# Optimization experiments

Hardware: AMD Instinct MI355X
Metric: run time of the kernel (lower is better)

The kernel has to match this reference:

```python
import jax, jax.numpy as jnp
import numpy as np

VOCAB_BLOCK = 2048
TEMP = 1.0
EPS_LO = 0.2
EPS_HI = 0.3


def setup_inputs() -> dict:
    key = jax.random.key(0)
    k = jax.random.split(key, 6)
    B, S, D, V = 4, 1024, 2048, 32768
    hidden_states = jax.random.normal(k[0], (B, S, D), dtype=jnp.float32)
    # 0.02 init scale keeps logits O(1) so exp/logsumexp stay well-conditioned
    lm_head_kernel = jax.random.normal(k[1], (D, V), dtype=jnp.float32) * 0.02
    input_ids = jax.random.randint(k[2], (B, S), 0, V, dtype=jnp.int32)
    labels = jax.random.randint(k[3], (B, S), 0, 2, dtype=jnp.int32)
    advantages = jax.random.normal(k[4], (B,), dtype=jnp.float32)
    old_per_token_logps = jax.random.normal(k[5], (B, S - 1), dtype=jnp.float32) * 0.1
    return {
        "hidden_states": hidden_states,
        "lm_head_kernel": lm_head_kernel,
        "input_ids": input_ids,
        "labels": labels,
        "advantages": advantages,
        "old_per_token_logps": old_per_token_logps,
    }


def _fused_logps(h, kernel):
    """Streaming logsumexp over vocab blocks; never materializes [B,T,V]."""
    B, T, D = h.shape
    V = kernel.shape[1]
    nb = V // VOCAB_BLOCK
    Wb = kernel.reshape(D, nb, VOCAB_BLOCK).transpose(1, 0, 2)  # [nb, D, bs]

    def step(carry, wb):
        m, s = carry
        lg = jnp.einsum("btd,dv->btv", h, wb) / TEMP  # [B,T,bs]
        bm = lg.max(axis=-1)
        nm = jnp.maximum(m, bm)
        s = s * jnp.exp(m - nm) + jnp.exp(lg - nm[..., None]).sum(axis=-1)
        return (nm, s), None

    init = (jnp.full((B, T), -jnp.inf, dtype=h.dtype), jnp.zeros((B, T), dtype=h.dtype))
    (m, s), _ = jax.lax.scan(step, init, Wb)
    return m + jnp.log(s)  # logsumexp over full vocab, [B,T]


def reference(hidden_states, lm_head_kernel, input_ids, labels, advantages, old_per_token_logps):
    h = hidden_states[:, :-1, :]            # [B,T,D], T = S-1
    chosen = input_ids[:, 1:]               # [B,T]
    mask = labels[:, 1:].astype(jnp.float32)

    # chosen-token logit: gather kernel columns, no full logits tensor
    w_sel = lm_head_kernel.T[chosen]        # [B,T,D]
    chosen_logit = jnp.einsum("btd,btd->bt", h, w_sel) / TEMP

    lse = _fused_logps(h, lm_head_kernel)
    per_token_logps = chosen_logit - lse    # [B,T]

    ratio = jnp.exp(per_token_logps - old_per_token_logps)
    adv = advantages[:, None]
    loss1 = ratio * adv
    loss2 = jnp.clip(ratio, 1.0 - EPS_LO, 1.0 + EPS_HI) * adv
    per_token_loss = -jnp.minimum(loss1, loss2)

    total_valid = mask.sum()
    loss = (per_token_loss * mask).sum() / total_valid
    return loss, jax.lax.stop_gradient(per_token_logps)
```

## Files before the change

### kernel.cpp

```cpp
#include <hip/hip_runtime.h>
#include <hip/hip_bf16.h>

typedef unsigned short u16;
typedef unsigned char u8;
typedef unsigned long long u64;
typedef __attribute__((ext_vector_type(4))) int i32x4;
typedef __attribute__((ext_vector_type(8))) int i32x8;
typedef __attribute__((ext_vector_type(4))) float f32x4;

#define NROWS 4092
#define NROWS_PAD 4096
#define DDIM 2048
#define VDIM 32768
#define NCHUNK 512
#define SC8 0x7F7F7F7F
#define BUFB 65536u

__device__ __forceinline__ u8 f2fp8(float f) {
  union { float f; unsigned u; } v; v.f = f;
  unsigned s = (v.u >> 24) & 0x80u;
  unsigned a = v.u & 0x7FFFFFFFu;
  if (a >= 0x43E80000u) return (u8)(s | 0x7E);
  int e = (int)(a >> 23) - 127;
  unsigned m = a & 0x7FFFFFu;
  if (e < -6) {
    unsigned full = m | 0x800000u;
    int sh = 20 + (-6 - e);
    if (sh > 31) return (u8)s;
    unsigned q = full >> sh;
    unsigned rem = full & ((1u << sh) - 1u), half = 1u << (sh - 1);
    q += (rem > half || (rem == half && (q & 1u)));
    return (u8)(s | q);
  }
  unsigned q = m >> 20, rem = m & 0xFFFFFu;
  q += (rem > 0x80000u || (rem == 0x80000u && (q & 1u)));
  unsigned bits = (((unsigned)(e + 7)) << 3) + q;
  if (bits >= 0x7Fu) bits = 0x7Eu;
  return (u8)(s | bits);
}

__device__ __forceinline__ void gload16(const void* g, void* l) {
  using gp_t = const __attribute__((address_space(1))) unsigned*;
  using lp_t = __attribute__((address_space(3))) unsigned*;
  __builtin_amdgcn_global_load_lds((gp_t)g, (lp_t)(unsigned)(unsigned long long)l,
                                   16, 0, 0);
}

#define BAR() __builtin_amdgcn_s_barrier()
#define SB()  __builtin_amdgcn_sched_barrier(0)
#define SHUF(a, b) __builtin_shufflevector(a, b, 0, 1, 2, 3, 4, 5, 6, 7)

__global__ void init_k(const int* __restrict__ ids, int* __restrict__ chosen,
                       float* __restrict__ chlog, float* __restrict__ accum) {
  int i = blockIdx.x * 256 + threadIdx.x;
  if (i < NROWS_PAD) {
    int v = -1;
    if (i < NROWS) { int b = i / 1023, t = i % 1023; v = ids[b * 1024 + t + 1]; }
    chosen[i] = v;
    chlog[i] = 0.f;
  }
  if (i < 2) accum[i] = 0.f;
}

__global__ void bucket_k(const int* __restrict__ chosen,
                         int* __restrict__ boff, int* __restrict__ bent) {
  __shared__ int cnt[512];
  __shared__ int base[512];
  int tid = threadIdx.x;
  cnt[tid] = 0;
  __syncthreads();
  int loc[8], tile[8];
#pragma unroll
  for (int j = 0; j < 8; ++j) {
    int r = tid + (j << 9);
    int c = chosen[r];
    int ti = (c < 0) ? 512 : (c >> 6);
    tile[j] = ti;
    loc[j] = (ti < 512) ? atomicAdd(&cnt[ti], 1) : 0;
  }
  __syncthreads();
  if (tid == 0) {
    int s = 0;
    for (int i = 0; i < 512; ++i) { base[i] = s; s += cnt[i]; }
  }
  __syncthreads();
  boff[tid] = base[tid];
  if (tid == 511) boff[512] = base[511] + cnt[511];
#pragma unroll
  for (int j = 0; j < 8; ++j) {
    int r = tid + (j << 9);
    if (tile[j] < 512) bent[base[tile[j]] + loc[j]] = (r << 6) | (chosen[r] & 63);
  }
}

__global__ void conv_h(const float* __restrict__ hs, u8* __restrict__ h8) {
  int idx = blockIdx.x * 256 + threadIdx.x;
  int row = idx >> 8;
  int c8 = (idx & 255) << 3;
  u64 o = 0;
  if (row < NROWS) {
    int b = row / 1023, t = row % 1023;
    const float* p = hs + (size_t)((b << 10) + t) * DDIM + c8;
    float4 x = *(const float4*)p, y = *(const float4*)(p + 4);
    o = (u64)f2fp8(x.x * 16.f)        | ((u64)f2fp8(x.y * 16.f) << 8) |
        ((u64)f2fp8(x.z * 16.f) << 16) | ((u64)f2fp8(x.w * 16.f) << 24) |
        ((u64)f2fp8(y.x * 16.f) << 32) | ((u64)f2fp8(y.y * 16.f) << 40) |
        ((u64)f2fp8(y.z * 16.f) << 48) | ((u64)f2fp8(y.w * 16.f) << 56);
  }
  *(u64*)(h8 + (size_t)row * DDIM + c8) = o;
}

__global__ void transpose_w(const float* __restrict__ W, u8* __restrict__ WT8,
                            const float* __restrict__ hs,
                            const int* __restrict__ boff,
                            const int* __restrict__ bent,
                            float* __restrict__ chlog) {
  __shared__ __align__(16) float t32[64][68];
  __shared__ __align__(16) u8 t8[64][68];
  int v0 = blockIdx.x << 6, d0 = blockIdx.y << 6;
  int tid = threadIdx.x;
  int vi = (tid & 15) << 2, dl = tid >> 4;
#pragma unroll
  for (int i = 0; i < 4; ++i) {
    int d = dl + (i << 4);
    float4 w = *(const float4*)(W + (size_t)(d0 + d) * VDIM + v0 + vi);
    *(float4*)&t32[d][vi] = w;
    unsigned p = (unsigned)f2fp8(w.x * 64.f) |
                 ((unsigned)f2fp8(w.y * 64.f) << 8) |
                 ((unsigned)f2fp8(w.z * 64.f) << 16) |
                 ((unsigned)f2fp8(w.w * 64.f) << 24);
    *(unsigned*)&t8[d][vi] = p;
  }
  __syncthreads();
  int m0 = boff[blockIdx.x], m1 = boff[blockIdx.x + 1];
  int lane = tid & 63, wv = tid >> 6;
  for (int m = m0 + wv; m < m1; m += 4) {
    int e = bent[m];
    int r = e >> 6, cv = e & 63;
    int b = r / 1023, tt = r % 1023;
    float s = hs[(size_t)((b << 10) + tt) * DDIM + d0 + lane] * t32[lane][cv];
#pragma unroll
    for (int o = 1; o < 64; o <<= 1) s += __shfl_xor(s, o, 64);
    if (lane == 0) atomicAdd(chlog + r, s);
  }
  int vr = tid >> 2, dc = (tid & 3) << 4;
  union { u8 b[16]; ulonglong2 q; } u;
#pragma unroll
  for (int k = 0; k < 16; ++k) u.b[k] = t8[dc + k][vr];
  *(ulonglong2*)(WT8 + (size_t)(v0 + vr) * DDIM + d0 + dc) = u.q;
}

__global__ __launch_bounds__(512, 2) void gemm_lse(
    const u8* __restrict__ A, const u8* __restrict__ Bt,
    float2* __restrict__ partials) {
  extern __shared__ u16 smem[];
  char* lds = (char*)smem;

  const int tid = threadIdx.x;
  const int l = tid & 63;
  const int wid = tid >> 6;
  const int wm = wid >> 2, wn = wid & 3;
  const int ln = l & 15;
  const int g4 = l >> 4;
  const int xr = ln & 7;

  int bid = blockIdx.x;
  int id = ((bid & 7) << 8) | (bid >> 3);
  int bm = id & 15;
  int bn = id >> 4;
  const int m0 = bm << 8, n0 = bn << 8;

  const u8* Ab = A + (size_t)m0 * DDIM;
  const u8* Bb = Bt + (size_t)n0 * DDIM;

  const unsigned aA0 = (unsigned)((wm << 14) + (ln << 7)) + (((0 | g4) ^ xr) << 4);
  const unsigned aA1 = (unsigned)((wm << 14) + (ln << 7)) + (((4 | g4) ^ xr) << 4);
  const unsigned aB0 = 32768u + (unsigned)((wn << 13) + (ln << 7)) + (((0 | g4) ^ xr) << 4);
  const unsigned aB1 = 32768u + (unsigned)((wn << 13) + (ln << 7)) + (((4 | g4) ^ xr) << 4);

  const int srow = l >> 3;
  const unsigned selb = (unsigned)(((l & 7) ^ srow) << 4);
  unsigned voff[4];
#pragma unroll
  for (int j = 0; j < 4; ++j)
    voff[j] = (unsigned)(((((j << 3) + wid) << 3) | srow) * 2048) + selb;

#define RFL(x) __builtin_amdgcn_readfirstlane((int)(x))
#define GLL(src, dst) gload16((src), lds + RFL(dst))
#define LD4(off) (*(const i32x4*)(lds + (off)))
#define FRAG(b0, b1, o) SHUF(LD4((b0) + (o)), LD4((b1) + (o)))
#define DSTA(j) (unsigned)((((j) << 3) + wid) << 10)
#define DSTB(j) (32768u + (unsigned)((((j) << 3) + wid) << 10))

  f32x4 acc[8][4] = {};

#pragma unroll
  for (int j = 0; j < 4; ++j) GLL(Ab + voff[j], DSTA(j));
#pragma unroll
  for (int j = 0; j < 4; ++j) GLL(Bb + voff[j], DSTB(j));
  asm volatile("s_waitcnt vmcnt(0)" ::: "memory"); SB();
  BAR();
  SB();

  for (int t = 0; t < 16; ++t) {
    const unsigned fb = (unsigned)(t & 1) * BUFB;
    const unsigned fbn = BUFB - fb;
    const u8* baseA = Ab + ((t + 1) << 7);
    const u8* baseB = Bb + ((t + 1) << 7);
    const unsigned rA0 = fb + aA0, rA1 = fb + aA1;
    const unsigned rB0 = fb + aB0, rB1 = fb + aB1;

    i32x8 af[8];
#pragma unroll
    for (int mi = 0; mi < 8; ++mi) af[mi] = FRAG(rA0, rA1, mi * 2048);

#pragma unroll
    for (int ni = 0; ni < 4; ++ni) {
      i32x8 bf = FRAG(rB0, rB1, ni * 2048);
      if (t < 15) {
        if (ni == 0)      { GLL(baseA + voff[0], fbn + DSTA(0));
                            GLL(baseA + voff[1], fbn + DSTA(1)); }
        else if (ni == 1) { GLL(baseA + voff[2], fbn + DSTA(2));
                            GLL(baseA + voff[3], fbn + DSTA(3)); }
        else if (ni == 2) { GLL(baseB + voff[0], fbn + DSTB(0));
                            GLL(baseB + voff[1], fbn + DSTB(1)); }
        else              { GLL(baseB + voff[2], fbn + DSTB(2));
                            GLL(baseB + voff[3], fbn + DSTB(3)); }
      }
      __builtin_amdgcn_s_setprio(1);
#pragma unroll
      for (int mi = 0; mi < 8; ++mi)
        acc[mi][ni] = __builtin_amdgcn_mfma_scale_f32_16x16x128_f8f6f4(
            af[mi], bf, acc[mi][ni], 0, 0, 0, SC8, 0, SC8);
      __builtin_amdgcn_s_setprio(0);
    }
    if (t < 15) { asm volatile("s_waitcnt vmcnt(0)" ::: "memory"); }
    SB();
    BAR();
    SB();
  }

  const int chunk = (bn << 2) | wn;
#pragma unroll
  for (int mi = 0; mi < 8; ++mi) {
#pragma unroll
    for (int rr = 0; rr < 4; ++rr) {
      const int row = m0 + (wm << 7) + (mi << 4) + (g4 << 2) + rr;
      float v0 = acc[mi][0][rr] * 0.0009765625f;
      float v1 = acc[mi][1][rr] * 0.0009765625f;
      float v2 = acc[mi][2][rr] * 0.0009765625f;
      float v3 = acc[mi][3][rr] * 0.0009765625f;
      float mx = fmaxf(fmaxf(v0, v1), fmaxf(v2, v3));
#pragma unroll
      for (int o = 1; o < 16; o <<= 1) mx = fmaxf(mx, __shfl_xor(mx, o, 64));
      float s = __expf(v0 - mx) + __expf(v1 - mx) + __expf(v2 - mx) + __expf(v3 - mx);
#pragma unroll
      for (int o = 1; o < 16; o <<= 1) s += __shfl_xor(s, o, 64);
      if (ln == 0) partials[(size_t)row * NCHUNK + chunk] = make_float2(mx, s);
    }
  }
#undef DSTA
#undef DSTB
#undef FRAG
#undef LD4
#undef GLL
#undef RFL
}

__global__ void reduce_lse(const float2* __restrict__ partials,
                           const float* __restrict__ chlog,
                           const float* __restrict__ oldlp,
                           const int* __restrict__ labels,
                           const float* __restrict__ adv,
                           float* __restrict__ out, float* __restrict__ accum) {
  const int wid = threadIdx.x >> 6, l = threadIdx.x & 63;
  const int row = blockIdx.x * 4 + wid;
  float M = -INFINITY, S = 0.f;
  for (int c = l; c < NCHUNK; c += 64) {
    float2 p = partials[(size_t)row * NCHUNK + c];
    float Mn = fmaxf(M, p.x);
    S = S * __expf(M - Mn) + p.y * __expf(p.x - Mn);
    M = Mn;
  }
#pragma unroll
  for (int o = 1; o < 64; o <<= 1) {
    float Mo = __shfl_xor(M, o, 64), So = __shfl_xor(S, o, 64);
    float Mn = fmaxf(M, Mo);
    S = S * __expf(M - Mn) + So * __expf(Mo - Mn);
    M = Mn;
  }
  if (l == 0) {
    float lse = M + __logf(S);
    float ptl = chlog[row] - lse;
    out[1 + row] = ptl;
    int b = row / 1023, t = row % 1023;
    float a = adv[b];
    float ratio = __expf(ptl - oldlp[row]);
    float l1 = ratio * a;
    float l2 = fminf(fmaxf(ratio, 0.8f), 1.3f) * a;
    float mk = (float)labels[b * 1024 + t + 1];
    atomicAdd(accum + 0, -fminf(l1, l2) * mk);
    atomicAdd(accum + 1, mk);
  }
}

__global__ void finalize_k(const float* __restrict__ accum, float* __restrict__ out) {
  out[0] = accum[0] / accum[1];
}

extern "C" void kernel_launch(void* const* d_in, const int* in_sizes, int n_in,
                              void* d_out, int out_size, void* d_ws, size_t ws_size,
                              hipStream_t stream) {
  const float* hs     = (const float*)d_in[0];
  const float* W      = (const float*)d_in[1];
  const int*   ids    = (const int*)d_in[2];
  const int*   labels = (const int*)d_in[3];
  const float* adv    = (const float*)d_in[4];
  const float* oldlp  = (const float*)d_in[5];
  float* out = (float*)d_out;

  char* ws = (char*)d_ws;
  u8*     WT8      = (u8*)ws;
  u8*     h8       = (u8*)(ws + 67108864);
  float2* partials = (float2*)(ws + 75497472);
  float*  chlog    = (float*)(ws + 92274688);
  int*    chosen   = (int*)(ws + 92291072);
  float*  accum    = (float*)(ws + 92307456);
  int*    boff     = (int*)(ws + 92307520);
  int*    bent     = (int*)(ws + 92309632);

  (void)hipFuncSetAttribute((const void*)gemm_lse,
                            hipFuncAttributeMaxDynamicSharedMemorySize, 131072);

  init_k<<<16, 256, 0, stream>>>(ids, chosen, chlog, accum);
  bucket_k<<<1, 512, 0, stream>>>(chosen, boff, bent);
  conv_h<<<4096, 256, 0, stream>>>(hs, h8);
  transpose_w<<<dim3(512, 32), 256, 0, stream>>>(W, WT8, hs, boff, bent, chlog);
  gemm_lse<<<2048, 512, 131072, stream>>>(h8, WT8, partials);
  reduce_lse<<<1023, 256, 0, stream>>>(partials, chlog, oldlp, labels, adv, out, accum);
  finalize_k<<<1, 1, 0, stream>>>(accum, out);
}
```

Baseline: 506.5 us.

## Load B fragments directly from global into registers, halving LDS use

The GEMM no longer stages the B (weight) tile through LDS. Each wave loads its B fragments straight from global memory into registers with a one-step software prefetch, and only the A tile stays double-buffered in LDS. Dynamic shared memory drops from 128KB to 64KB, which may allow more resident blocks, and the wait is relaxed to vmcnt(8). The cost is uncoalesced, partly cache-dependent global loads in the MFMA inner loop, and a possible correctness risk if the loose wait count does not match how many loads are outstanding.

```diff
diff --git a/kernel.cpp b/kernel.cpp
--- a/kernel.cpp
+++ b/kernel.cpp
@@ -14,7 +14,6 @@
 #define VDIM 32768
 #define NCHUNK 512
 #define SC8 0x7F7F7F7F
-#define BUFB 65536u
 
 __device__ __forceinline__ u8 f2fp8(float f) {
   union { float f; unsigned u; } v; v.f = f;
@@ -171,12 +170,9 @@
   const int m0 = bm << 8, n0 = bn << 8;
 
   const u8* Ab = A + (size_t)m0 * DDIM;
-  const u8* Bb = Bt + (size_t)n0 * DDIM;
 
   const unsigned aA0 = (unsigned)((wm << 14) + (ln << 7)) + (((0 | g4) ^ xr) << 4);
   const unsigned aA1 = (unsigned)((wm << 14) + (ln << 7)) + (((4 | g4) ^ xr) << 4);
-  const unsigned aB0 = 32768u + (unsigned)((wn << 13) + (ln << 7)) + (((0 | g4) ^ xr) << 4);
-  const unsigned aB1 = 32768u + (unsigned)((wn << 13) + (ln << 7)) + (((4 | g4) ^ xr) << 4);
 
   const int srow = l >> 3;
   const unsigned selb = (unsigned)(((l & 7) ^ srow) << 4);
@@ -184,57 +180,54 @@
 #pragma unroll
   for (int j = 0; j < 4; ++j)
     voff[j] = (unsigned)(((((j << 3) + wid) << 3) | srow) * 2048) + selb;
+
+  const u8* bB = Bt + (size_t)(n0 + (wn << 6) + ln) * DDIM + (g4 << 4);
 
 #define RFL(x) __builtin_amdgcn_readfirstlane((int)(x))
 #define GLL(src, dst) gload16((src), lds + RFL(dst))
 #define LD4(off) (*(const i32x4*)(lds + (off)))
 #define FRAG(b0, b1, o) SHUF(LD4((b0) + (o)), LD4((b1) + (o)))
 #define DSTA(j) (unsigned)((((j) << 3) + wid) << 10)
-#define DSTB(j) (32768u + (unsigned)((((j) << 3) + wid) << 10))
+#define BLOAD(p) SHUF(*(const i32x4*)(p), *(const i32x4*)((p) + 64))
 
   f32x4 acc[8][4] = {};
 
 #pragma unroll
   for (int j = 0; j < 4; ++j) GLL(Ab + voff[j], DSTA(j));
-#pragma unroll
-  for (int j = 0; j < 4; ++j) GLL(Bb + voff[j], DSTB(j));
   asm volatile("s_waitcnt vmcnt(0)" ::: "memory"); SB();
   BAR();
   SB();
 
+  i32x8 bfC = BLOAD(bB);
+
   for (int t = 0; t < 16; ++t) {
-    const unsigned fb = (unsigned)(t & 1) * BUFB;
-    const unsigned fbn = BUFB - fb;
+    const unsigned fb = (unsigned)(t & 1) << 15;
+    const unsigned fbn = 32768u - fb;
     const u8* baseA = Ab + ((t + 1) << 7);
-    const u8* baseB = Bb + ((t + 1) << 7);
+    if (t < 15) {
+      GLL(baseA + voff[0], fbn + DSTA(0)); GLL(baseA + voff[1], fbn + DSTA(1));
+      GLL(baseA + voff[2], fbn + DSTA(2)); GLL(baseA + voff[3], fbn + DSTA(3));
+    }
+
     const unsigned rA0 = fb + aA0, rA1 = fb + aA1;
-    const unsigned rB0 = fb + aB0, rB1 = fb + aB1;
-
     i32x8 af[8];
 #pragma unroll
     for (int mi = 0; mi < 8; ++mi) af[mi] = FRAG(rA0, rA1, mi * 2048);
 
+    const u8* bT = bB + (t << 7);
 #pragma unroll
     for (int ni = 0; ni < 4; ++ni) {
-      i32x8 bf = FRAG(rB0, rB1, ni * 2048);
-      if (t < 15) {
-        if (ni == 0)      { GLL(baseA + voff[0], fbn + DSTA(0));
-                            GLL(baseA + voff[1], fbn + DSTA(1)); }
-        else if (ni == 1) { GLL(baseA + voff[2], fbn + DSTA(2));
-                            GLL(baseA + voff[3], fbn + DSTA(3)); }
-        else if (ni == 2) { GLL(baseB + voff[0], fbn + DSTB(0));
-                            GLL(baseB + voff[1], fbn + DSTB(1)); }
-        else              { GLL(baseB + voff[2], fbn + DSTB(2));
-                            GLL(baseB + voff[3], fbn + DSTB(3)); }
-      }
+      const u8* nb = (ni < 3) ? (bT + (ni + 1) * 32768) : (bT + 128);
+      i32x8 bfN = BLOAD(nb);
       __builtin_amdgcn_s_setprio(1);
 #pragma unroll
       for (int mi = 0; mi < 8; ++mi)
         acc[mi][ni] = __builtin_amdgcn_mfma_scale_f32_16x16x128_f8f6f4(
-            af[mi], bf, acc[mi][ni], 0, 0, 0, SC8, 0, SC8);
+            af[mi], bfC, acc[mi][ni], 0, 0, 0, SC8, 0, SC8);
       __builtin_amdgcn_s_setprio(0);
+      bfC = bfN;
     }
-    if (t < 15) { asm volatile("s_waitcnt vmcnt(0)" ::: "memory"); }
+    if (t < 15) { asm volatile("s_waitcnt vmcnt(8)" ::: "memory"); }
     SB();
     BAR();
     SB();
@@ -260,7 +253,7 @@
     }
   }
 #undef DSTA
-#undef DSTB
+#undef BLOAD
 #undef FRAG
 #undef LD4
 #undef GLL
@@ -330,13 +323,13 @@
   int*    bent     = (int*)(ws + 92309632);
 
   (void)hipFuncSetAttribute((const void*)gemm_lse,
-                            hipFuncAttributeMaxDynamicSharedMemorySize, 131072);
+                            hipFuncAttributeMaxDynamicSharedMemorySize, 65536);
 
   init_k<<<16, 256, 0, stream>>>(ids, chosen, chlog, accum);
   bucket_k<<<1, 512, 0, stream>>>(chosen, boff, bent);
   conv_h<<<4096, 256, 0, stream>>>(hs, h8);
   transpose_w<<<dim3(512, 32), 256, 0, stream>>>(W, WT8, hs, boff, bent, chlog);
-  gemm_lse<<<2048, 512, 131072, stream>>>(h8, WT8, partials);
+  gemm_lse<<<2048, 512, 65536, stream>>>(h8, WT8, partials);
   reduce_lse<<<1023, 256, 0, stream>>>(partials, chlog, oldlp, labels, adv, out, accum);
   finalize_k<<<1, 1, 0, stream>>>(accum, out);
 }
```

Measured after the change: 602.5 us. 19.0% more time.
